# Performance work log

Measured on AMD Instinct MI355X. Metric: run time of the kernel, lower is better.

## Reference

```python
import jax, jax.numpy as jnp
import numpy as np

SR = 48000.0
HARMONIC_NUM = 8
DIM = HARMONIC_NUM + 1
SINE_AMP = 0.1
NOISE_STD = 0.003
VOICED_THRESHOLD = 0.0
B, T, UPP = 8, 512, 512


def setup_inputs() -> dict:
    key = jax.random.key(0)
    k1, k2, k3, k4 = jax.random.split(key, 4)
    f0 = jax.random.uniform(k1, (B, T), minval=100.0, maxval=400.0)
    voiced = (jax.random.uniform(k2, (B, T)) > 0.2).astype(jnp.float32)
    f0 = f0 * voiced  # some unvoiced (f0 == 0) frames
    rand_ini = jax.random.uniform(k3, (B, DIM)).at[:, 0].set(0.0)
    noise_randn = jax.random.normal(k4, (B, T * UPP, DIM), dtype=jnp.float32)
    return {"f0": f0, "rand_ini": rand_ini, "noise_randn": noise_randn, "upp": UPP}


def _linear_upsample_ac(x, upp):
    # x: [B, T, D] -> [B, T*upp, D]; torch F.interpolate(mode='linear', align_corners=True)
    b, t, d = x.shape
    L = t * upp
    pos = jnp.arange(L, dtype=x.dtype) * (t - 1) / (L - 1)
    i0 = jnp.clip(jnp.floor(pos).astype(jnp.int32), 0, t - 2)
    frac = (pos - i0.astype(x.dtype))[None, :, None]
    return x[:, i0] * (1.0 - frac) + x[:, i0 + 1] * frac


def reference(f0, rand_ini, noise_randn, upp):
    # harmonics: fundamental * (1..DIM)
    mult = jnp.arange(1, DIM + 1, dtype=f0.dtype)
    f0_buf = f0[:, :, None] * mult                      # [B, T, DIM]
    rad = (f0_buf / SR) % 1.0                           # normalized per-frame phase increment
    rad = rad.at[:, 0, :].add(rand_ini)                 # random initial phase (0 for fundamental)

    # frame-rate cumulative phase, linearly upsampled (align_corners=True), wrapped
    tmp = jnp.cumsum(rad, axis=1) * upp
    tmp = _linear_upsample_ac(tmp, upp) % 1.0           # [B, L, DIM]

    # sample-rate phase increments via nearest upsampling
    rad_up = jnp.repeat(rad, upp, axis=1) % 1.0         # [B, L, DIM]

    # -1 shift wherever wrapped phase decreases (wrap correction)
    wrap = (tmp[:, 1:] - tmp[:, :-1] < 0).astype(rad_up.dtype)
    shift = jnp.concatenate([jnp.zeros_like(rad_up[:, :1]), -wrap], axis=1)

    phase = jnp.cumsum(rad_up + shift, axis=1)
    sine_waves = jnp.sin(2.0 * np.pi * phase) * SINE_AMP

    uv = (f0 > VOICED_THRESHOLD).astype(f0.dtype)[:, :, None]  # [B, T, 1]
    uv = jnp.repeat(uv, upp, axis=1)                            # [B, L, 1]

    noise_amp = uv * NOISE_STD + (1.0 - uv) * (SINE_AMP / 3.0)
    noise = noise_amp * noise_randn
    sine_waves = sine_waves * uv + noise
    return sine_waves, uv, noise
```

## Files before the change

### kernel.cpp

```cpp
#include <hip/hip_runtime.h>
#include <math.h>

#define BB 8
#define TT 512
#define DIMN 9
#define UPP 512
#define LL (TT * UPP)
#define TOTAL (BB * LL * DIMN)
#define SRATE 48000.0

__device__ __forceinline__ double dfrac(double x) { return x - floor(x); }

__global__ void frame_scan_kernel(const float* __restrict__ f0,
                                  const float* __restrict__ rand_ini,
                                  float* __restrict__ rp_out,
                                  float* __restrict__ cf_out) {
    const int bd = blockIdx.x;
    const int b = bd / DIMN;
    const int d = bd % DIMN;
    const int t = threadIdx.x;

    double f = (double)f0[b * TT + t];
    double raw = f * (double)(d + 1) * (1.0 / SRATE);
    if (t == 0) raw += (double)rand_ini[b * DIMN + d];
    double rp = dfrac(raw);
    rp_out[(b * TT + t) * DIMN + d] = (float)rp;

    __shared__ double sh[TT];
    sh[t] = (double)UPP * rp;
    __syncthreads();
    for (int off = 1; off < TT; off <<= 1) {
        double add = (t >= off) ? sh[t - off] : 0.0;
        __syncthreads();
        sh[t] += add;
        __syncthreads();
    }
    double C = (t == 0) ? 0.0 : sh[t - 1];
    cf_out[(b * TT + t) * DIMN + d] = (float)dfrac(C);
}

__global__ void uv_kernel(const float* __restrict__ f0, float* __restrict__ out1) {
    unsigned i4 = (blockIdx.x * blockDim.x + threadIdx.x) * 4u;
    unsigned b = i4 >> 18;
    unsigned l = i4 & (LL - 1u);
    unsigned t = l >> 9;
    float uvf = (f0[b * TT + t] > 0.0f) ? 1.0f : 0.0f;
    float4 v = make_float4(uvf, uvf, uvf, uvf);
    *reinterpret_cast<float4*>(out1 + i4) = v;
}

__global__ void __launch_bounds__(256) sine_out_kernel(
        const float* __restrict__ f0,
        const float* __restrict__ noise_randn,
        const float* __restrict__ rp,
        const float* __restrict__ cf,
        float* __restrict__ out0,
        float* __restrict__ out2) {
    unsigned base = (blockIdx.x * blockDim.x + threadIdx.x) * 4u;

    float4 nz4 = *reinterpret_cast<const float4*>(noise_randn + base);
    const float* nzp = &nz4.x;

    unsigned d  = base % 9u;
    unsigned bl = base / 9u;

    float o0[4], o2[4];
#pragma unroll
    for (int j = 0; j < 4; ++j) {
        unsigned b = bl >> 18;
        unsigned l = bl & (LL - 1u);
        unsigned t = l >> 9;
        unsigned k = l & 511u;
        unsigned fidx = (b * TT + t) * DIMN + d;

        float r = rp[fidx];
        float c = cf[fidx];
        float ph = fmaf((float)(k + 1), r, c);
        float ff = __builtin_amdgcn_fractf(ph);
        float s  = __builtin_amdgcn_sinf(ff) * 0.1f;

        float f0v = f0[b * TT + t];
        bool  v   = f0v > 0.0f;
        float nz  = (v ? 0.003f : (0.1f / 3.0f)) * nzp[j];
        o0[j] = (v ? s : 0.0f) + nz;
        o2[j] = nz;

        if (++d == 9u) { d = 0u; ++bl; }
    }
    *reinterpret_cast<float4*>(out0 + base) = make_float4(o0[0], o0[1], o0[2], o0[3]);
    *reinterpret_cast<float4*>(out2 + base) = make_float4(o2[0], o2[1], o2[2], o2[3]);
}

extern "C" void kernel_launch(void* const* d_in, const int* in_sizes, int n_in,
                              void* d_out, int out_size, void* d_ws, size_t ws_size,
                              hipStream_t stream) {
    const float* f0          = (const float*)d_in[0];
    const float* rand_ini    = (const float*)d_in[1];
    const float* noise_randn = (const float*)d_in[2];

    float* rp = (float*)d_ws;
    float* cf = rp + (size_t)BB * TT * DIMN;

    float* out0 = (float*)d_out;
    float* out1 = out0 + (size_t)BB * LL * DIMN;
    float* out2 = out1 + (size_t)BB * LL;

    frame_scan_kernel<<<BB * DIMN, TT, 0, stream>>>(f0, rand_ini, rp, cf);

    const int block = 256;
    const unsigned grid2 = TOTAL / 4 / block;
    sine_out_kernel<<<grid2, block, 0, stream>>>(f0, noise_randn, rp, cf, out0, out2);

    const unsigned grid3 = (BB * LL) / 4 / block;
    uv_kernel<<<grid3, block, 0, stream>>>(f0, out1);
}
```

Before: 47.61 us.

## Use wave-level shuffle scan for frame phases and fuse uv write into sine kernel

The frame scan now gives each (batch, harmonic) pair a single 64-lane wavefront. Each lane does a serial prefix over 8 frames, and the lanes are combined with a shuffle-up scan in double precision. This replaces the 512-thread shared-memory scan and its many block barriers. The separate uv kernel is removed and its broadcast writes are folded into the sine/noise kernel, which saves one launch at the cost of some divergent extra work in the first part of that grid. The double-precision shuffles and the strided rp/cf stores remain.

```diff
diff --git a/kernel.cpp b/kernel.cpp
--- a/kernel.cpp
+++ b/kernel.cpp
@@ -11,42 +11,47 @@
 
 __device__ __forceinline__ double dfrac(double x) { return x - floor(x); }
 
-__global__ void frame_scan_kernel(const float* __restrict__ f0,
-                                  const float* __restrict__ rand_ini,
-                                  float* __restrict__ rp_out,
-                                  float* __restrict__ cf_out) {
-    const int bd = blockIdx.x;
-    const int b = bd / DIMN;
-    const int d = bd % DIMN;
-    const int t = threadIdx.x;
+__global__ void __launch_bounds__(256) frame_scan_wave(
+        const float* __restrict__ f0,
+        const float* __restrict__ rand_ini,
+        float* __restrict__ rp_out,
+        float* __restrict__ cf_out) {
+    const int wave = blockIdx.x * 4 + (threadIdx.x >> 6);
+    const int lane = threadIdx.x & 63;
+    if (wave >= BB * DIMN) return;
+    const int b = wave / DIMN;
+    const int d = wave % DIMN;
+    const int t0 = lane * 8;
 
-    double f = (double)f0[b * TT + t];
-    double raw = f * (double)(d + 1) * (1.0 / SRATE);
-    if (t == 0) raw += (double)rand_ini[b * DIMN + d];
-    double rp = dfrac(raw);
-    rp_out[(b * TT + t) * DIMN + d] = (float)rp;
+    float4 fA = *reinterpret_cast<const float4*>(f0 + b * TT + t0);
+    float4 fB = *reinterpret_cast<const float4*>(f0 + b * TT + t0 + 4);
+    float fv[8] = {fA.x, fA.y, fA.z, fA.w, fB.x, fB.y, fB.z, fB.w};
 
-    __shared__ double sh[TT];
-    sh[t] = (double)UPP * rp;
-    __syncthreads();
-    for (int off = 1; off < TT; off <<= 1) {
-        double add = (t >= off) ? sh[t - off] : 0.0;
-        __syncthreads();
-        sh[t] += add;
-        __syncthreads();
+    const double mult = (double)(d + 1) * (1.0 / SRATE);
+    double rpj[8], pex[8];
+    double s = 0.0;
+#pragma unroll
+    for (int j = 0; j < 8; ++j) {
+        double raw = (double)fv[j] * mult;
+        if (lane == 0 && j == 0) raw += (double)rand_ini[b * DIMN + d];
+        double rp = dfrac(raw);
+        rpj[j] = rp;
+        pex[j] = s;
+        s += (double)UPP * rp;
     }
-    double C = (t == 0) ? 0.0 : sh[t - 1];
-    cf_out[(b * TT + t) * DIMN + d] = (float)dfrac(C);
-}
-
-__global__ void uv_kernel(const float* __restrict__ f0, float* __restrict__ out1) {
-    unsigned i4 = (blockIdx.x * blockDim.x + threadIdx.x) * 4u;
-    unsigned b = i4 >> 18;
-    unsigned l = i4 & (LL - 1u);
-    unsigned t = l >> 9;
-    float uvf = (f0[b * TT + t] > 0.0f) ? 1.0f : 0.0f;
-    float4 v = make_float4(uvf, uvf, uvf, uvf);
-    *reinterpret_cast<float4*>(out1 + i4) = v;
+    double incl = s;
+#pragma unroll
+    for (int off = 1; off < 64; off <<= 1) {
+        double up = __shfl_up(incl, off);
+        if (lane >= off) incl += up;
+    }
+    const double E = incl - s;
+#pragma unroll
+    for (int j = 0; j < 8; ++j) {
+        int fidx = (b * TT + t0 + j) * DIMN + d;
+        rp_out[fidx] = (float)rpj[j];
+        cf_out[fidx] = (float)dfrac(E + pex[j]);
+    }
 }
 
 __global__ void __launch_bounds__(256) sine_out_kernel(
@@ -55,8 +60,10 @@
         const float* __restrict__ rp,
         const float* __restrict__ cf,
         float* __restrict__ out0,
+        float* __restrict__ out1,
         float* __restrict__ out2) {
-    unsigned base = (blockIdx.x * blockDim.x + threadIdx.x) * 4u;
+    unsigned gid  = blockIdx.x * blockDim.x + threadIdx.x;
+    unsigned base = gid * 4u;
 
     float4 nz4 = *reinterpret_cast<const float4*>(noise_randn + base);
     const float* nzp = &nz4.x;
@@ -89,6 +96,15 @@
     }
     *reinterpret_cast<float4*>(out0 + base) = make_float4(o0[0], o0[1], o0[2], o0[3]);
     *reinterpret_cast<float4*>(out2 + base) = make_float4(o2[0], o2[1], o2[2], o2[3]);
+
+    if (gid < (BB * LL) / 4u) {
+        unsigned i4 = gid * 4u;
+        unsigned b = i4 >> 18;
+        unsigned l = i4 & (LL - 1u);
+        unsigned t = l >> 9;
+        float uvf = (f0[b * TT + t] > 0.0f) ? 1.0f : 0.0f;
+        *reinterpret_cast<float4*>(out1 + i4) = make_float4(uvf, uvf, uvf, uvf);
+    }
 }
 
 extern "C" void kernel_launch(void* const* d_in, const int* in_sizes, int n_in,
@@ -105,12 +121,10 @@
     float* out1 = out0 + (size_t)BB * LL * DIMN;
     float* out2 = out1 + (size_t)BB * LL;
 
-    frame_scan_kernel<<<BB * DIMN, TT, 0, stream>>>(f0, rand_ini, rp, cf);
+    frame_scan_wave<<<18, 256, 0, stream>>>(f0, rand_ini, rp, cf);
 
     const int block = 256;
     const unsigned grid2 = TOTAL / 4 / block;
-    sine_out_kernel<<<grid2, block, 0, stream>>>(f0, noise_randn, rp, cf, out0, out2);
-
-    const unsigned grid3 = (BB * LL) / 4 / block;
-    uv_kernel<<<grid3, block, 0, stream>>>(f0, out1);
+    sine_out_kernel<<<grid2, block, 0, stream>>>(f0, noise_randn, rp, cf,
+                                                 out0, out1, out2);
 }
```

Result: faster. 45.51 us (-4.4%).
